# Performance work log

Measured on AMD Instinct MI355X. Metric: run time of the kernel, lower is better.

The kernel has to match this reference:

```python
import jax, jax.numpy as jnp
import numpy as np

N = 100000      # num_nodes
E = 1600000     # num_edges (avg degree 16)
IN = 128        # in_channels
HID = 8         # hidden_channels (per head)
HEADS = 8
OUT = 64        # out_channels
NEG_SLOPE = 0.2


def setup_inputs() -> dict:
    key = jax.random.key(0)
    ks = jax.random.split(key, 11)
    s = 0.05
    return {
        "x": jax.random.normal(ks[0], (N, IN), jnp.float32),
        "edge_index": jax.random.randint(ks[1], (2, E), 0, N, dtype=jnp.int32),
        "W1": jax.random.normal(ks[2], (IN, HEADS * HID), jnp.float32) * s,
        "a_src1": jax.random.normal(ks[3], (HEADS, HID), jnp.float32) * s,
        "a_dst1": jax.random.normal(ks[4], (HEADS, HID), jnp.float32) * s,
        "b1": jnp.zeros((HEADS * HID,), jnp.float32),
        "W2": jax.random.normal(ks[5], (HEADS * HID, OUT), jnp.float32) * s,
        "a_src2": jax.random.normal(ks[6], (1, OUT), jnp.float32) * s,
        "a_dst2": jax.random.normal(ks[7], (1, OUT), jnp.float32) * s,
        "b2": jnp.zeros((OUT,), jnp.float32),
    }


def gat_conv(x, src, dst, W, a_src, a_dst, bias, heads, out_ch):
    """PyG GATConv (concat=True, dropout=0, self-loops already in src/dst)."""
    n = x.shape[0]
    h = (x @ W).reshape(n, heads, out_ch)               # [N, H, C]
    al_src = jnp.einsum('nhc,hc->nh', h, a_src)          # [N, H]
    al_dst = jnp.einsum('nhc,hc->nh', h, a_dst)          # [N, H]
    e = jax.nn.leaky_relu(al_src[src] + al_dst[dst], NEG_SLOPE)  # [E, H]
    # segment softmax over destination nodes (numerically stable)
    e_max = jax.ops.segment_max(e, dst, num_segments=n)  # [N, H]
    ex = jnp.exp(e - e_max[dst])
    denom = jax.ops.segment_sum(ex, dst, num_segments=n)
    alpha = ex / (denom[dst] + 1e-16)                    # [E, H]
    msg = h[src] * alpha[:, :, None]                     # [E, H, C]
    out = jax.ops.segment_sum(msg, dst, num_segments=n)  # [N, H, C]
    return out.reshape(n, heads * out_ch) + bias


def reference(x, edge_index, W1, a_src1, a_dst1, b1, W2, a_src2, a_dst2, b2):
    n = x.shape[0]
    loops = jnp.arange(n, dtype=edge_index.dtype)
    src = jnp.concatenate([edge_index[0], loops])        # add self-loops (PyG default)
    dst = jnp.concatenate([edge_index[1], loops])
    h = gat_conv(x, src, dst, W1, a_src1, a_dst1, b1, HEADS, HID)
    h = jax.nn.elu(h)
    out = gat_conv(h, src, dst, W2, a_src2, a_dst2, b2, 1, OUT)
    return out
```

## Files before the change

kernel.cpp:

```cpp
#include <hip/hip_runtime.h>
#include <hip/hip_bf16.h>

#define IN_CH   128
#define HEADS   8
#define HID     8
#define MID_CH  64
#define OUT_CH  64
#define CAP     64
#define NRANGE  8

typedef unsigned short u16;
__device__ __forceinline__ u16 f2bu(float f) {
    union { float f; unsigned int i; } v; v.f = f;
    unsigned int lsb = (v.i >> 16) & 1u;
    return (u16)((v.i + 0x7fffu + lsb) >> 16);
}
__device__ __forceinline__ float2 up2(unsigned int u) {
    union { unsigned int i; float f; } a, b;
    a.i = u << 16; b.i = u & 0xffff0000u;
    return make_float2(a.f, b.f);
}
__device__ __forceinline__ float lrelu(float e) { return (e > 0.f) ? e : 0.2f * e; }

__global__ __launch_bounds__(256) void k1_fill(
    const int* __restrict__ src, const int* __restrict__ dst,
    int* __restrict__ deg, int* __restrict__ adj, int E, int N) {
    int range = blockIdx.x & (NRANGE - 1);
    int chunk = blockIdx.x >> 3;
    int lo = (int)(((long long)N * range) >> 3);
    int hi = (int)(((long long)N * (range + 1)) >> 3);
    int t = chunk * 256 + threadIdx.x;
    int base = t * 4;
    if (base + 3 < E) {
        int4 d4 = *(const int4*)(dst + base);
        bool ix = (d4.x >= lo && d4.x < hi);
        bool iy = (d4.y >= lo && d4.y < hi);
        bool iz = (d4.z >= lo && d4.z < hi);
        bool iw = (d4.w >= lo && d4.w < hi);
        if (ix | iy | iz | iw) {
            int4 s4 = *(const int4*)(src + base);
            if (ix) { int p = atomicAdd(&deg[d4.x], 1); if (p < CAP) adj[d4.x * CAP + p] = s4.x; }
            if (iy) { int p = atomicAdd(&deg[d4.y], 1); if (p < CAP) adj[d4.y * CAP + p] = s4.y; }
            if (iz) { int p = atomicAdd(&deg[d4.z], 1); if (p < CAP) adj[d4.z * CAP + p] = s4.z; }
            if (iw) { int p = atomicAdd(&deg[d4.w], 1); if (p < CAP) adj[d4.w * CAP + p] = s4.w; }
        }
    } else {
        for (int j = 0; j < 4; j++) {
            int e = base + j;
            if (e < E) {
                int d = dst[e];
                if (d >= lo && d < hi) {
                    int p = atomicAdd(&deg[d], 1);
                    if (p < CAP) adj[d * CAP + p] = src[e];
                }
            }
        }
    }
}

__global__ __launch_bounds__(256) void k2_gemm1(
    const float* __restrict__ x, const float* __restrict__ W1,
    const float* __restrict__ a_src, const float* __restrict__ a_dst,
    u16* __restrict__ h1b, float* __restrict__ als, float* __restrict__ ald, int N)
{
    __shared__ float Wl[IN_CH * MID_CH];
    int tid = threadIdx.x;
    {
        const float4* W4 = (const float4*)W1;
        float4* Wl4 = (float4*)Wl;
        for (int i = tid; i < IN_CH * MID_CH / 4; i += 256) Wl4[i] = W4[i];
    }
    __syncthreads();

    int wave = tid >> 6, lane = tid & 63;
    int base = blockIdx.x * 16;
    int r0 = wave * 4;
    int n0 = base + r0;
    int c0 = (n0 + 0 < N) ? (n0 + 0) : (N - 1);
    int c1 = (n0 + 1 < N) ? (n0 + 1) : (N - 1);
    int c2 = (n0 + 2 < N) ? (n0 + 2) : (N - 1);
    int c3 = (n0 + 3 < N) ? (n0 + 3) : (N - 1);
    const float* xr0 = x + (size_t)__builtin_amdgcn_readfirstlane(c0) * IN_CH;
    const float* xr1 = x + (size_t)__builtin_amdgcn_readfirstlane(c1) * IN_CH;
    const float* xr2 = x + (size_t)__builtin_amdgcn_readfirstlane(c2) * IN_CH;
    const float* xr3 = x + (size_t)__builtin_amdgcn_readfirstlane(c3) * IN_CH;

    float acc[4] = {0.f, 0.f, 0.f, 0.f};
    #pragma unroll 16
    for (int k = 0; k < IN_CH; k++) {
        float w = Wl[k * MID_CH + lane];
        acc[0] = fmaf(xr0[k], w, acc[0]);
        acc[1] = fmaf(xr1[k], w, acc[1]);
        acc[2] = fmaf(xr2[k], w, acc[2]);
        acc[3] = fmaf(xr3[k], w, acc[3]);
    }
    float asv = a_src[lane];
    float adv = a_dst[lane];
    #pragma unroll
    for (int g = 0; g < 4; g++) {
        int n = n0 + g;
        if (n >= N) continue;
        h1b[(size_t)n * MID_CH + lane] = f2bu(acc[g]);
        float vs = acc[g] * asv;
        float vd = acc[g] * adv;
        vs += __shfl_xor(vs, 1); vs += __shfl_xor(vs, 2); vs += __shfl_xor(vs, 4);
        vd += __shfl_xor(vd, 1); vd += __shfl_xor(vd, 2); vd += __shfl_xor(vd, 4);
        if ((lane & 7) == 0) {
            als[n * HEADS + (lane >> 3)] = vs;
            ald[n * HEADS + (lane >> 3)] = vd;
        }
    }
}

__global__ __launch_bounds__(256) void k3_agg1(
    const int* __restrict__ deg, const int* __restrict__ adj,
    const u16* __restrict__ h1b, const float* __restrict__ als,
    const float* __restrict__ ald, const float* __restrict__ b1,
    float* __restrict__ h2, int N)
{
    __shared__ int adjl[4][CAP];
    int wave = threadIdx.x >> 6, lane = threadIdx.x & 63;
    int n = blockIdx.x * 4 + wave;
    bool valid = (n < N);
    int nc = valid ? n : (N - 1);

    int g = lane >> 3;
    int c8 = lane & 7;
    int dg = deg[nc]; if (dg > CAP) dg = CAP;
    if (lane < dg) adjl[wave][lane] = adj[(size_t)nc * CAP + lane];
    float aldv = ald[nc * HEADS + c8];
    __syncthreads();

    const uint4* h1v = (const uint4*)h1b;
    float acc[8] = {0,0,0,0,0,0,0,0};
    float denom = 0.f;
    for (int i = g; i < dg; i += 8) {
        int s = adjl[wave][i];
        float ex = __expf(lrelu(als[s * HEADS + c8] + aldv));
        uint4 q = h1v[(size_t)s * 8 + c8];
        float2 p0 = up2(q.x), p1 = up2(q.y), p2 = up2(q.z), p3 = up2(q.w);
        denom += ex;
        acc[0] += ex * p0.x; acc[1] += ex * p0.y;
        acc[2] += ex * p1.x; acc[3] += ex * p1.y;
        acc[4] += ex * p2.x; acc[5] += ex * p2.y;
        acc[6] += ex * p3.x; acc[7] += ex * p3.y;
    }
    if (g == 0) {
        float ex = __expf(lrelu(als[nc * HEADS + c8] + aldv));
        uint4 q = h1v[(size_t)nc * 8 + c8];
        float2 p0 = up2(q.x), p1 = up2(q.y), p2 = up2(q.z), p3 = up2(q.w);
        denom += ex;
        acc[0] += ex * p0.x; acc[1] += ex * p0.y;
        acc[2] += ex * p1.x; acc[3] += ex * p1.y;
        acc[4] += ex * p2.x; acc[5] += ex * p2.y;
        acc[6] += ex * p3.x; acc[7] += ex * p3.y;
    }
    denom += __shfl_xor(denom, 8); denom += __shfl_xor(denom, 16); denom += __shfl_xor(denom, 32);
    #pragma unroll
    for (int j = 0; j < 8; j++) {
        acc[j] += __shfl_xor(acc[j], 8);
        acc[j] += __shfl_xor(acc[j], 16);
        acc[j] += __shfl_xor(acc[j], 32);
    }
    float inv = 1.f / (denom + 1e-16f);

    if (g == 0 && valid) {
        const float4* b4 = (const float4*)b1;
        float4 bl = b4[c8 * 2], bh = b4[c8 * 2 + 1];
        float4 o0, o1;
        o0.x = acc[0] * inv + bl.x; o0.y = acc[1] * inv + bl.y;
        o0.z = acc[2] * inv + bl.z; o0.w = acc[3] * inv + bl.w;
        o1.x = acc[4] * inv + bh.x; o1.y = acc[5] * inv + bh.y;
        o1.z = acc[6] * inv + bh.z; o1.w = acc[7] * inv + bh.w;
        o0.x = (o0.x > 0.f) ? o0.x : (__expf(o0.x) - 1.f);
        o0.y = (o0.y > 0.f) ? o0.y : (__expf(o0.y) - 1.f);
        o0.z = (o0.z > 0.f) ? o0.z : (__expf(o0.z) - 1.f);
        o0.w = (o0.w > 0.f) ? o0.w : (__expf(o0.w) - 1.f);
        o1.x = (o1.x > 0.f) ? o1.x : (__expf(o1.x) - 1.f);
        o1.y = (o1.y > 0.f) ? o1.y : (__expf(o1.y) - 1.f);
        o1.z = (o1.z > 0.f) ? o1.z : (__expf(o1.z) - 1.f);
        o1.w = (o1.w > 0.f) ? o1.w : (__expf(o1.w) - 1.f);
        float4* h2v = (float4*)h2;
        h2v[(size_t)n * 16 + c8 * 2]     = o0;
        h2v[(size_t)n * 16 + c8 * 2 + 1] = o1;
    }
}

__global__ __launch_bounds__(256) void k4_gemm2(
    const float* __restrict__ h2, const float* __restrict__ W2,
    const float* __restrict__ a_src, const float* __restrict__ a_dst,
    u16* __restrict__ t2b, float* __restrict__ als, float* __restrict__ ald, int N)
{
    __shared__ float Wl[MID_CH * OUT_CH];
    int tid = threadIdx.x;
    {
        const float4* W4 = (const float4*)W2;
        float4* Wl4 = (float4*)Wl;
        for (int i = tid; i < MID_CH * OUT_CH / 4; i += 256) Wl4[i] = W4[i];
    }
    __syncthreads();

    int wave = tid >> 6, lane = tid & 63;
    int base = blockIdx.x * 16;
    int r0 = wave * 4;
    int n0 = base + r0;
    int c0 = (n0 + 0 < N) ? (n0 + 0) : (N - 1);
    int c1 = (n0 + 1 < N) ? (n0 + 1) : (N - 1);
    int c2 = (n0 + 2 < N) ? (n0 + 2) : (N - 1);
    int c3 = (n0 + 3 < N) ? (n0 + 3) : (N - 1);
    const float* xr0 = h2 + (size_t)__builtin_amdgcn_readfirstlane(c0) * MID_CH;
    const float* xr1 = h2 + (size_t)__builtin_amdgcn_readfirstlane(c1) * MID_CH;
    const float* xr2 = h2 + (size_t)__builtin_amdgcn_readfirstlane(c2) * MID_CH;
    const float* xr3 = h2 + (size_t)__builtin_amdgcn_readfirstlane(c3) * MID_CH;

    float acc[4] = {0.f, 0.f, 0.f, 0.f};
    #pragma unroll 16
    for (int k = 0; k < MID_CH; k++) {
        float w = Wl[k * OUT_CH + lane];
        acc[0] = fmaf(xr0[k], w, acc[0]);
        acc[1] = fmaf(xr1[k], w, acc[1]);
        acc[2] = fmaf(xr2[k], w, acc[2]);
        acc[3] = fmaf(xr3[k], w, acc[3]);
    }
    float asv = a_src[lane];
    float adv = a_dst[lane];
    #pragma unroll
    for (int g = 0; g < 4; g++) {
        int n = n0 + g;
        if (n >= N) continue;
        t2b[(size_t)n * OUT_CH + lane] = f2bu(acc[g]);
        float vs = acc[g] * asv;
        float vd = acc[g] * adv;
        #pragma unroll
        for (int off = 1; off < 64; off <<= 1) {
            vs += __shfl_xor(vs, off);
            vd += __shfl_xor(vd, off);
        }
        if (lane == 0) { als[n] = vs; ald[n] = vd; }
    }
}

__global__ __launch_bounds__(256) void k5_agg2(
    const int* __restrict__ deg, const int* __restrict__ adj,
    const u16* __restrict__ t2b, const float* __restrict__ als,
    const float* __restrict__ ald, const float* __restrict__ b2,
    float* __restrict__ out, int N)
{
    __shared__ int adjl[4][CAP];
    int wave = threadIdx.x >> 6, lane = threadIdx.x & 63;
    int n = blockIdx.x * 4 + wave;
    bool valid = (n < N);
    int nc = valid ? n : (N - 1);

    int g = lane >> 3;
    int c8 = lane & 7;
    int dg = deg[nc]; if (dg > CAP) dg = CAP;
    if (lane < dg) adjl[wave][lane] = adj[(size_t)nc * CAP + lane];
    float aldv = ald[nc];
    __syncthreads();

    const uint4* t2v = (const uint4*)t2b;
    float acc[8] = {0,0,0,0,0,0,0,0};
    float denom = 0.f;
    for (int i = g; i < dg; i += 8) {
        int s = adjl[wave][i];
        float ex = __expf(lrelu(als[s] + aldv));
        uint4 q = t2v[(size_t)s * 8 + c8];
        float2 p0 = up2(q.x), p1 = up2(q.y), p2 = up2(q.z), p3 = up2(q.w);
        denom += ex;
        acc[0] += ex * p0.x; acc[1] += ex * p0.y;
        acc[2] += ex * p1.x; acc[3] += ex * p1.y;
        acc[4] += ex * p2.x; acc[5] += ex * p2.y;
        acc[6] += ex * p3.x; acc[7] += ex * p3.y;
    }
    if (g == 0) {
        float ex = __expf(lrelu(als[nc] + aldv));
        uint4 q = t2v[(size_t)nc * 8 + c8];
        float2 p0 = up2(q.x), p1 = up2(q.y), p2 = up2(q.z), p3 = up2(q.w);
        denom += ex;
        acc[0] += ex * p0.x; acc[1] += ex * p0.y;
        acc[2] += ex * p1.x; acc[3] += ex * p1.y;
        acc[4] += ex * p2.x; acc[5] += ex * p2.y;
        acc[6] += ex * p3.x; acc[7] += ex * p3.y;
    }
    denom += __shfl_xor(denom, 8); denom += __shfl_xor(denom, 16); denom += __shfl_xor(denom, 32);
    #pragma unroll
    for (int j = 0; j < 8; j++) {
        acc[j] += __shfl_xor(acc[j], 8);
        acc[j] += __shfl_xor(acc[j], 16);
        acc[j] += __shfl_xor(acc[j], 32);
    }
    float inv = 1.f / (denom + 1e-16f);

    if (g == 0 && valid) {
        const float4* b4 = (const float4*)b2;
        float4 bl = b4[c8 * 2], bh = b4[c8 * 2 + 1];
        float4 o0, o1;
        o0.x = acc[0] * inv + bl.x; o0.y = acc[1] * inv + bl.y;
        o0.z = acc[2] * inv + bl.z; o0.w = acc[3] * inv + bl.w;
        o1.x = acc[4] * inv + bh.x; o1.y = acc[5] * inv + bh.y;
        o1.z = acc[6] * inv + bh.z; o1.w = acc[7] * inv + bh.w;
        float4* ov = (float4*)out;
        ov[(size_t)n * 16 + c8 * 2]     = o0;
        ov[(size_t)n * 16 + c8 * 2 + 1] = o1;
    }
}

extern "C" void kernel_launch(void* const* d_in, const int* in_sizes, int n_in,
                              void* d_out, int out_size, void* d_ws, size_t ws_size,
                              hipStream_t stream) {
    const float* x   = (const float*)d_in[0];
    const int*   ei  = (const int*)d_in[1];
    const float* W1  = (const float*)d_in[2];
    const float* as1 = (const float*)d_in[3];
    const float* ad1 = (const float*)d_in[4];
    const float* b1  = (const float*)d_in[5];
    const float* W2  = (const float*)d_in[6];
    const float* as2 = (const float*)d_in[7];
    const float* ad2 = (const float*)d_in[8];
    const float* b2  = (const float*)d_in[9];
    float* out = (float*)d_out;

    int N = in_sizes[0] / IN_CH;
    int E = in_sizes[1] / 2;
    const int* srcp = ei;
    const int* dstp = ei + E;

    char* w = (char*)d_ws;
    size_t off = 0;
    auto alloc = [&](size_t bytes) {
        void* p = w + off;
        off += (bytes + 255) & ~(size_t)255;
        return p;
    };
    int*   deg  = (int*)  alloc((size_t)N * 4);
    int*   adj  = (int*)  alloc((size_t)N * CAP * 4);
    u16*   h1b  = (u16*)  alloc((size_t)N * MID_CH * 2);
    float* als1 = (float*)alloc((size_t)N * HEADS * 4);
    float* ald1 = (float*)alloc((size_t)N * HEADS * 4);
    float* h2   = (float*)alloc((size_t)N * MID_CH * 4);
    u16*   t2b  = (u16*)  alloc((size_t)N * OUT_CH * 2);
    float* als2 = (float*)alloc((size_t)N * 4);
    float* ald2 = (float*)alloc((size_t)N * 4);
    (void)ws_size; (void)n_in; (void)out_size;

    hipMemsetAsync(deg, 0, (size_t)N * 4, stream);
    int chunks = (E + 1023) / 1024;
    k1_fill<<<chunks * NRANGE, 256, 0, stream>>>(srcp, dstp, deg, adj, E, N);
    k2_gemm1<<<(N + 15) / 16, 256, 0, stream>>>(x, W1, as1, ad1, h1b, als1, ald1, N);
    k3_agg1<<<(N + 3) / 4, 256, 0, stream>>>(deg, adj, h1b, als1, ald1, b1, h2, N);
    k4_gemm2<<<(N + 15) / 16, 256, 0, stream>>>(h2, W2, as2, ad2, t2b, als2, ald2, N);
    k5_agg2<<<(N + 3) / 4, 256, 0, stream>>>(deg, adj, t2b, als2, ald2, b2, out, N);
}
```

Measured before the change: 387.6 us.

## Fuse adjacency fill with GEMM1 and stage x rows in LDS for GEMMs

Merges the edge-bucketing fill kernel and the first projection GEMM into one launch. Blocks are interleaved so GEMM and scatter work run concurrently, which removes one launch and lets atomic-bound scatter overlap compute. Both GEMM kernels now stage 32 input rows in shared memory and give each wave 8 rows, raising reuse of each W load. The cost is more LDS per block (48KB for the fused kernel), which may cut occupancy for the scatter blocks that do not use it.

Result: slower. 1.503 ms (+287.6%).

```diff
diff --git a/kernel.cpp b/kernel.cpp
--- a/kernel.cpp
+++ b/kernel.cpp
@@ -7,7 +7,6 @@
 #define MID_CH  64
 #define OUT_CH  64
 #define CAP     64
-#define NRANGE  8
 
 typedef unsigned short u16;
 __device__ __forceinline__ u16 f2bu(float f) {
@@ -22,92 +21,120 @@
 }
 __device__ __forceinline__ float lrelu(float e) { return (e > 0.f) ? e : 0.2f * e; }
 
-__global__ __launch_bounds__(256) void k1_fill(
+__global__ __launch_bounds__(256) void k12_fused(
     const int* __restrict__ src, const int* __restrict__ dst,
-    int* __restrict__ deg, int* __restrict__ adj, int E, int N) {
-    int range = blockIdx.x & (NRANGE - 1);
-    int chunk = blockIdx.x >> 3;
-    int lo = (int)(((long long)N * range) >> 3);
-    int hi = (int)(((long long)N * (range + 1)) >> 3);
-    int t = chunk * 256 + threadIdx.x;
-    int base = t * 4;
-    if (base + 3 < E) {
-        int4 d4 = *(const int4*)(dst + base);
-        bool ix = (d4.x >= lo && d4.x < hi);
-        bool iy = (d4.y >= lo && d4.y < hi);
-        bool iz = (d4.z >= lo && d4.z < hi);
-        bool iw = (d4.w >= lo && d4.w < hi);
-        if (ix | iy | iz | iw) {
-            int4 s4 = *(const int4*)(src + base);
-            if (ix) { int p = atomicAdd(&deg[d4.x], 1); if (p < CAP) adj[d4.x * CAP + p] = s4.x; }
-            if (iy) { int p = atomicAdd(&deg[d4.y], 1); if (p < CAP) adj[d4.y * CAP + p] = s4.y; }
-            if (iz) { int p = atomicAdd(&deg[d4.z], 1); if (p < CAP) adj[d4.z * CAP + p] = s4.z; }
-            if (iw) { int p = atomicAdd(&deg[d4.w], 1); if (p < CAP) adj[d4.w * CAP + p] = s4.w; }
-        }
-    } else {
-        for (int j = 0; j < 4; j++) {
-            int e = base + j;
-            if (e < E) {
-                int d = dst[e];
-                if (d >= lo && d < hi) {
-                    int p = atomicAdd(&deg[d], 1);
-                    if (p < CAP) adj[d * CAP + p] = src[e];
-                }
-            }
-        }
-    }
-}
-
-__global__ __launch_bounds__(256) void k2_gemm1(
+    int* __restrict__ deg, int* __restrict__ adj,
     const float* __restrict__ x, const float* __restrict__ W1,
     const float* __restrict__ a_src, const float* __restrict__ a_dst,
-    u16* __restrict__ h1b, float* __restrict__ als, float* __restrict__ ald, int N)
+    u16* __restrict__ h1b, float* __restrict__ als, float* __restrict__ ald,
+    int E, int N)
 {
     __shared__ float Wl[IN_CH * MID_CH];
-    int tid = threadIdx.x;
-    {
-        const float4* W4 = (const float4*)W1;
-        float4* Wl4 = (float4*)Wl;
-        for (int i = tid; i < IN_CH * MID_CH / 4; i += 256) Wl4[i] = W4[i];
-    }
-    __syncthreads();
-
-    int wave = tid >> 6, lane = tid & 63;
-    int base = blockIdx.x * 16;
-    int r0 = wave * 4;
-    int n0 = base + r0;
-    int c0 = (n0 + 0 < N) ? (n0 + 0) : (N - 1);
-    int c1 = (n0 + 1 < N) ? (n0 + 1) : (N - 1);
-    int c2 = (n0 + 2 < N) ? (n0 + 2) : (N - 1);
-    int c3 = (n0 + 3 < N) ? (n0 + 3) : (N - 1);
-    const float* xr0 = x + (size_t)__builtin_amdgcn_readfirstlane(c0) * IN_CH;
-    const float* xr1 = x + (size_t)__builtin_amdgcn_readfirstlane(c1) * IN_CH;
-    const float* xr2 = x + (size_t)__builtin_amdgcn_readfirstlane(c2) * IN_CH;
-    const float* xr3 = x + (size_t)__builtin_amdgcn_readfirstlane(c3) * IN_CH;
-
-    float acc[4] = {0.f, 0.f, 0.f, 0.f};
-    #pragma unroll 16
-    for (int k = 0; k < IN_CH; k++) {
-        float w = Wl[k * MID_CH + lane];
-        acc[0] = fmaf(xr0[k], w, acc[0]);
-        acc[1] = fmaf(xr1[k], w, acc[1]);
-        acc[2] = fmaf(xr2[k], w, acc[2]);
-        acc[3] = fmaf(xr3[k], w, acc[3]);
-    }
-    float asv = a_src[lane];
-    float adv = a_dst[lane];
-    #pragma unroll
-    for (int g = 0; g < 4; g++) {
-        int n = n0 + g;
-        if (n >= N) continue;
-        h1b[(size_t)n * MID_CH + lane] = f2bu(acc[g]);
-        float vs = acc[g] * asv;
-        float vd = acc[g] * adv;
-        vs += __shfl_xor(vs, 1); vs += __shfl_xor(vs, 2); vs += __shfl_xor(vs, 4);
-        vd += __shfl_xor(vd, 1); vd += __shfl_xor(vd, 2); vd += __shfl_xor(vd, 4);
-        if ((lane & 7) == 0) {
-            als[n * HEADS + (lane >> 3)] = vs;
-            ald[n * HEADS + (lane >> 3)] = vd;
+    __shared__ float xl[32 * IN_CH];
+
+    int b = blockIdx.x;
+    int g = b >> 3, r = b & 7;
+    int chunks = (E + 1023) >> 10;
+    int ngemm  = (N + 31) >> 5;
+    int gg     = (ngemm + 7) >> 3;
+    int T      = chunks + gg;
+    int t1 = (int)(((long long)g * gg) / T);
+    int t2 = (int)(((long long)(g + 1) * gg) / T);
+
+    if (t2 != t1) {
+        int gb = t1 * 8 + r;
+        if (gb >= ngemm) return;
+        int tid = threadIdx.x;
+        {
+            const float4* W4 = (const float4*)W1;
+            float4* Wl4 = (float4*)Wl;
+            #pragma unroll
+            for (int i = tid; i < IN_CH * MID_CH / 4; i += 256) Wl4[i] = W4[i];
+        }
+        int base = gb * 32;
+        {
+            float4* xl4 = (float4*)xl;
+            const float4* x4 = (const float4*)x;
+            #pragma unroll
+            for (int i = tid; i < 32 * IN_CH / 4; i += 256) {
+                int rr = i >> 5;
+                int n = base + rr;
+                xl4[i] = (n < N) ? x4[(size_t)n * (IN_CH / 4) + (i & 31)]
+                                 : make_float4(0.f, 0.f, 0.f, 0.f);
+            }
+        }
+        __syncthreads();
+
+        int wave = tid >> 6, lane = tid & 63;
+        int r0 = wave * 8;
+        float acc[8] = {0, 0, 0, 0, 0, 0, 0, 0};
+        #pragma unroll
+        for (int kc = 0; kc < IN_CH; kc += 4) {
+            float4 xv[8];
+            #pragma unroll
+            for (int q = 0; q < 8; q++)
+                xv[q] = *(const float4*)&xl[(r0 + q) * IN_CH + kc];
+            #pragma unroll
+            for (int kk = 0; kk < 4; kk++) {
+                float w = Wl[(kc + kk) * MID_CH + lane];
+                const float xk0 = ((const float*)&xv[0])[kk];
+                acc[0] = fmaf(xk0, w, acc[0]);
+                acc[1] = fmaf(((const float*)&xv[1])[kk], w, acc[1]);
+                acc[2] = fmaf(((const float*)&xv[2])[kk], w, acc[2]);
+                acc[3] = fmaf(((const float*)&xv[3])[kk], w, acc[3]);
+                acc[4] = fmaf(((const float*)&xv[4])[kk], w, acc[4]);
+                acc[5] = fmaf(((const float*)&xv[5])[kk], w, acc[5]);
+                acc[6] = fmaf(((const float*)&xv[6])[kk], w, acc[6]);
+                acc[7] = fmaf(((const float*)&xv[7])[kk], w, acc[7]);
+            }
+        }
+        float asv = a_src[lane];
+        float adv = a_dst[lane];
+        #pragma unroll
+        for (int q = 0; q < 8; q++) {
+            int n = base + r0 + q;
+            if (n >= N) continue;
+            h1b[(size_t)n * MID_CH + lane] = f2bu(acc[q]);
+            float vs = acc[q] * asv;
+            float vd = acc[q] * adv;
+            vs += __shfl_xor(vs, 1); vs += __shfl_xor(vs, 2); vs += __shfl_xor(vs, 4);
+            vd += __shfl_xor(vd, 1); vd += __shfl_xor(vd, 2); vd += __shfl_xor(vd, 4);
+            if ((lane & 7) == 0) {
+                als[n * HEADS + (lane >> 3)] = vs;
+                ald[n * HEADS + (lane >> 3)] = vd;
+            }
+        }
+    } else {
+        int chunk = g - t1;
+        int range = r;
+        int lo = (int)(((long long)N * range) >> 3);
+        int hi = (int)(((long long)N * (range + 1)) >> 3);
+        int t = chunk * 256 + threadIdx.x;
+        int base = t * 4;
+        if (base + 3 < E) {
+            int4 d4 = *(const int4*)(dst + base);
+            bool ix = (d4.x >= lo && d4.x < hi);
+            bool iy = (d4.y >= lo && d4.y < hi);
+            bool iz = (d4.z >= lo && d4.z < hi);
+            bool iw = (d4.w >= lo && d4.w < hi);
+            if (ix | iy | iz | iw) {
+                int4 s4 = *(const int4*)(src + base);
+                if (ix) { int p = atomicAdd(&deg[d4.x], 1); if (p < CAP) adj[d4.x * CAP + p] = s4.x; }
+                if (iy) { int p = atomicAdd(&deg[d4.y], 1); if (p < CAP) adj[d4.y * CAP + p] = s4.y; }
+                if (iz) { int p = atomicAdd(&deg[d4.z], 1); if (p < CAP) adj[d4.z * CAP + p] = s4.z; }
+                if (iw) { int p = atomicAdd(&deg[d4.w], 1); if (p < CAP) adj[d4.w * CAP + p] = s4.w; }
+            }
+        } else {
+            for (int j = 0; j < 4; j++) {
+                int e = base + j;
+                if (e < E) {
+                    int d = dst[e];
+                    if (d >= lo && d < hi) {
+                        int p = atomicAdd(&deg[d], 1);
+                        if (p < CAP) adj[d * CAP + p] = src[e];
+                    }
+                }
+            }
         }
     }
 }
@@ -192,45 +219,59 @@
     u16* __restrict__ t2b, float* __restrict__ als, float* __restrict__ ald, int N)
 {
     __shared__ float Wl[MID_CH * OUT_CH];
+    __shared__ float xl[32 * MID_CH];
     int tid = threadIdx.x;
     {
         const float4* W4 = (const float4*)W2;
         float4* Wl4 = (float4*)Wl;
+        #pragma unroll
         for (int i = tid; i < MID_CH * OUT_CH / 4; i += 256) Wl4[i] = W4[i];
     }
+    int base = blockIdx.x * 32;
+    {
+        float4* xl4 = (float4*)xl;
+        const float4* x4 = (const float4*)h2;
+        #pragma unroll
+        for (int i = tid; i < 32 * MID_CH / 4; i += 256) {
+            int rr = i >> 4;
+            int n = base + rr;
+            xl4[i] = (n < N) ? x4[(size_t)n * (MID_CH / 4) + (i & 15)]
+                             : make_float4(0.f, 0.f, 0.f, 0.f);
+        }
+    }
     __syncthreads();
 
     int wave = tid >> 6, lane = tid & 63;
-    int base = blockIdx.x * 16;
-    int r0 = wave * 4;
-    int n0 = base + r0;
-    int c0 = (n0 + 0 < N) ? (n0 + 0) : (N - 1);
-    int c1 = (n0 + 1 < N) ? (n0 + 1) : (N - 1);
-    int c2 = (n0 + 2 < N) ? (n0 + 2) : (N - 1);
-    int c3 = (n0 + 3 < N) ? (n0 + 3) : (N - 1);
-    const float* xr0 = h2 + (size_t)__builtin_amdgcn_readfirstlane(c0) * MID_CH;
-    const float* xr1 = h2 + (size_t)__builtin_amdgcn_readfirstlane(c1) * MID_CH;
-    const float* xr2 = h2 + (size_t)__builtin_amdgcn_readfirstlane(c2) * MID_CH;
-    const float* xr3 = h2 + (size_t)__builtin_amdgcn_readfirstlane(c3) * MID_CH;
-
-    float acc[4] = {0.f, 0.f, 0.f, 0.f};
-    #pragma unroll 16
-    for (int k = 0; k < MID_CH; k++) {
-        float w = Wl[k * OUT_CH + lane];
-        acc[0] = fmaf(xr0[k], w, acc[0]);
-        acc[1] = fmaf(xr1[k], w, acc[1]);
-        acc[2] = fmaf(xr2[k], w, acc[2]);
-        acc[3] = fmaf(xr3[k], w, acc[3]);
+    int r0 = wave * 8;
+    float acc[8] = {0, 0, 0, 0, 0, 0, 0, 0};
+    #pragma unroll
+    for (int kc = 0; kc < MID_CH; kc += 4) {
+        float4 xv[8];
+        #pragma unroll
+        for (int q = 0; q < 8; q++)
+            xv[q] = *(const float4*)&xl[(r0 + q) * MID_CH + kc];
+        #pragma unroll
+        for (int kk = 0; kk < 4; kk++) {
+            float w = Wl[(kc + kk) * OUT_CH + lane];
+            acc[0] = fmaf(((const float*)&xv[0])[kk], w, acc[0]);
+            acc[1] = fmaf(((const float*)&xv[1])[kk], w, acc[1]);
+            acc[2] = fmaf(((const float*)&xv[2])[kk], w, acc[2]);
+            acc[3] = fmaf(((const float*)&xv[3])[kk], w, acc[3]);
+            acc[4] = fmaf(((const float*)&xv[4])[kk], w, acc[4]);
+            acc[5] = fmaf(((const float*)&xv[5])[kk], w, acc[5]);
+            acc[6] = fmaf(((const float*)&xv[6])[kk], w, acc[6]);
+            acc[7] = fmaf(((const float*)&xv[7])[kk], w, acc[7]);
+        }
     }
     float asv = a_src[lane];
     float adv = a_dst[lane];
     #pragma unroll
-    for (int g = 0; g < 4; g++) {
-        int n = n0 + g;
+    for (int q = 0; q < 8; q++) {
+        int n = base + r0 + q;
         if (n >= N) continue;
-        t2b[(size_t)n * OUT_CH + lane] = f2bu(acc[g]);
-        float vs = acc[g] * asv;
-        float vd = acc[g] * adv;
+        t2b[(size_t)n * OUT_CH + lane] = f2bu(acc[q]);
+        float vs = acc[q] * asv;
+        float vd = acc[q] * adv;
         #pragma unroll
         for (int off = 1; off < 64; off <<= 1) {
             vs += __shfl_xor(vs, off);
@@ -345,10 +386,14 @@
     (void)ws_size; (void)n_in; (void)out_size;
 
     hipMemsetAsync(deg, 0, (size_t)N * 4, stream);
-    int chunks = (E + 1023) / 1024;
-    k1_fill<<<chunks * NRANGE, 256, 0, stream>>>(srcp, dstp, deg, adj, E, N);
-    k2_gemm1<<<(N + 15) / 16, 256, 0, stream>>>(x, W1, as1, ad1, h1b, als1, ald1, N);
+
+    int chunks = (E + 1023) >> 10;
+    int ngemm  = (N + 31) >> 5;
+    int gg     = (ngemm + 7) >> 3;
+    int T      = chunks + gg;
+    k12_fused<<<T * 8, 256, 0, stream>>>(srcp, dstp, deg, adj,
+                                         x, W1, as1, ad1, h1b, als1, ald1, E, N);
     k3_agg1<<<(N + 3) / 4, 256, 0, stream>>>(deg, adj, h1b, als1, ald1, b1, h2, N);
-    k4_gemm2<<<(N + 15) / 16, 256, 0, stream>>>(h2, W2, as2, ad2, t2b, als2, ald2, N);
+    k4_gemm2<<<(N + 31) / 32, 256, 0, stream>>>(h2, W2, as2, ad2, t2b, als2, ald2, N);
     k5_agg2<<<(N + 3) / 4, 256, 0, stream>>>(deg, adj, t2b, als2, ald2, b2, out, N);
 }
```
